# Optimization experiments

Measured on AMD Instinct MI355X. Metric: run time of the kernel, lower is better.

Reference implementation:

```python
import jax, jax.numpy as jnp
import numpy as np

N = 4096      # nodes
F = 32        # num_features (GATConv in = out per head)
H = 2         # heads
NHID = 64     # per-branch mlp output
C = 10        # num_classes
J = 3         # wavelet filters
E = 65536     # edges (avg degree 16)
G = 13        # num_gat = (3**3 - 1) // 2
NEG_SLOPE = 0.2


def setup_inputs() -> dict:
    key = jax.random.key(0)
    ks = jax.random.split(key, 12)
    sc = np.float32(1.0 / np.sqrt(N))
    g = np.float32(0.1)
    x = jax.random.normal(ks[0], (N, F), jnp.float32)
    edge_index = jax.random.randint(ks[1], (2, E), 0, N)
    U = jax.random.normal(ks[2], (N, N), jnp.float32) * sc
    psi = jax.random.normal(ks[3], (J, N, N), jnp.float32) * sc
    # 13 GATConv(F, F, heads=H) parameter stacks
    gat_W = jax.random.normal(ks[4], (G, F, H * F), jnp.float32) * g
    att_src = jax.random.normal(ks[5], (G, H, F), jnp.float32) * g
    att_dst = jax.random.normal(ks[6], (G, H, F), jnp.float32) * g
    gat_b = jnp.zeros((G, H * F), jnp.float32)
    # 13 branch MLPs: Linear(H*F -> NHID)
    mlp_W = jax.random.normal(ks[7], (G, H * F, NHID), jnp.float32) * g
    mlp_b = jnp.zeros((G, NHID), jnp.float32)
    # final head: Linear(13*NHID -> C)
    out_W = jax.random.normal(ks[8], (G * NHID, C), jnp.float32) * g
    out_b = jnp.zeros((C,), jnp.float32)
    return {"x": x, "edge_index": edge_index, "U": U, "psi": psi,
            "gat_W": gat_W, "att_src": att_src, "att_dst": att_dst,
            "gat_b": gat_b, "mlp_W": mlp_W, "mlp_b": mlp_b,
            "out_W": out_W, "out_b": out_b}


def _gat_branch(coef, W, a_s, a_d, bg, mw, mb, src, dst):
    # GATConv(F, F, heads=H, concat=True) in eval mode, then ELU + Linear.
    h = (coef @ W).reshape(N, H, F)                       # [N,H,F]
    es = jnp.einsum('nhf,hf->nh', h, a_s)                 # src attention logits
    ed = jnp.einsum('nhf,hf->nh', h, a_d)                 # dst attention logits
    e = jax.nn.leaky_relu(es[src] + ed[dst], NEG_SLOPE)   # [E+N,H]
    m = jax.ops.segment_max(e, dst, num_segments=N)       # stable softmax per dst
    w = jnp.exp(e - m[dst])
    z = jax.ops.segment_sum(w, dst, num_segments=N)
    alpha = w / (z[dst] + 1e-16)
    out = jax.ops.segment_sum(alpha[:, :, None] * h[src], dst, num_segments=N)
    out = out.reshape(N, H * F) + bg
    return jax.nn.elu(out) @ mw + mb                      # branch MLP -> [N,NHID]


def reference(x, edge_index, U, psi, gat_W, att_src, att_dst, gat_b,
              mlp_W, mlp_b, out_W, out_b):
    loops = jnp.arange(N)
    src = jnp.concatenate([edge_index[0], loops])         # add_self_loops
    dst = jnp.concatenate([edge_index[1], loops])
    # Scattering tree (layer=3, J=3): 1 + 3 + 9 = 13 coefficient maps.
    af = jnp.abs(x)
    coef0 = U @ af                                        # [N,F]
    y1 = jnp.einsum('jnm,mf->jnf', psi, af)               # level-1 wavelets [J,N,F]
    a1 = jnp.abs(y1)
    coef1 = jnp.einsum('nm,jmf->jnf', U, a1)              # [J,N,F]
    y2 = jnp.einsum('knm,jmf->jknf', psi, a1)             # level-2: psi_k @ |y1_j|
    coef2 = jnp.einsum('nm,jkmf->jknf', U, jnp.abs(y2)).reshape(J * J, N, F)
    coefs = jnp.concatenate([coef0[None], coef1, coef2], axis=0)  # [13,N,F]
    branch = jax.vmap(lambda c, W, a_s, a_d, bg, mw, mb:
                      _gat_branch(c, W, a_s, a_d, bg, mw, mb, src, dst))
    yb = branch(coefs, gat_W, att_src, att_dst, gat_b, mlp_W, mlp_b)  # [13,N,NHID]
    feat = jnp.moveaxis(yb, 0, 1).reshape(N, G * NHID)    # concat branches per node
    logits = jax.nn.elu(feat) @ out_W + out_b             # [N,C]
    return jax.nn.log_softmax(logits, axis=1)
```

## Files before the change

kernel.cpp:

```cpp
#include <hip/hip_runtime.h>
#include <hip/hip_bf16.h>

#define NN 4096
#define FF 32
#define EE 65536
#define GG 13

typedef float floatx4 __attribute__((ext_vector_type(4)));
typedef __bf16 bf16x8 __attribute__((ext_vector_type(8)));
typedef short short8 __attribute__((ext_vector_type(8)));

__device__ inline unsigned short f2bf(float f) {
    unsigned u = __float_as_uint(f);
    u += 0x7FFFu + ((u >> 16) & 1u);
    return (unsigned short)(u >> 16);
}

__device__ inline void gl2lds16(const float* g, float* l) {
    __builtin_amdgcn_global_load_lds(
        (__attribute__((address_space(1))) void*)(void*)(g),
        (__attribute__((address_space(3))) void*)(l), 16, 0, 0);
}


__global__ void k_prep1(const float* __restrict__ x, unsigned short* __restrict__ B) {
    int tid = blockIdx.x * 256 + threadIdx.x;
    int k = tid >> 5, col = tid & 31;
    float v = fabsf(x[tid]);
    B[(((k >> 5) * 2 + (col >> 4)) << 9) + ((col & 15) << 5) + (k & 31)] = f2bf(v);
}

__global__ void k_prep2(const float* __restrict__ P1, unsigned short* __restrict__ B) {
    int tid = blockIdx.x * 256 + threadIdx.x;
    int k = tid / 96, jf = tid % 96;
    int j = jf >> 5, f = jf & 31;
    float v = fabsf(P1[((1 + j) * NN + k) * FF + f]);
    B[(((k >> 5) * 6 + (jf >> 4)) << 9) + ((jf & 15) << 5) + (k & 31)] = f2bf(v);
}

__global__ void k_prep3(const float* __restrict__ P2, unsigned short* __restrict__ B) {
    int tid = blockIdx.x * 256 + threadIdx.x;
    int k = tid / 288, cc = tid % 288;
    int k3 = cc / 96, jf = cc % 96;
    float v = fabsf(P2[((1 + k3) * NN + k) * 96 + jf]);
    B[(((k >> 5) * 18 + (cc >> 4)) << 9) + ((cc & 15) << 5) + (k & 31)] = f2bf(v);
}

__global__ __launch_bounds__(512, 8) void k_pass1(const float* __restrict__ Umat,
                                                  const float* __restrict__ Psi,
                                                  const unsigned short* __restrict__ Bfrag,
                                                  float* __restrict__ Pout,
                                                  unsigned short* __restrict__ Apack) {
    __shared__ float abuf[2][16 * 256];
    __shared__ float cs[2][16 * 32];
    int tile = blockIdx.x, mat = blockIdx.y;
    const float* A = (mat == 0) ? Umat : (Psi + (size_t)(mat - 1) * NN * NN);
    int tid = threadIdx.x;
    int wave = tid >> 6, lane = tid & 63;
    int c15 = lane & 15, q = lane >> 4;

    const float* atile = A + (size_t)tile * 16 * NN;
    const unsigned short* bbase = Bfrag + (c15 << 5) + (q << 3);
    unsigned short* apk = Apack + ((size_t)mat << 24) + (size_t)tile * 65536
                          + (c15 << 5) + (q << 3);

    int r0 = 2 * wave, r1 = 2 * wave + 1;
    const float* g0 = atile + (size_t)r0 * NN + ((lane ^ (r0 & 7)) << 2);
    const float* g1 = atile + (size_t)r1 * NN + ((lane ^ (r1 & 7)) << 2);
    float* l0 = &abuf[0][wave * 512];
    float* l1 = &abuf[1][wave * 512];

    int swz = c15 & 7;
    int u0 = ((wave * 8 + q * 2 + 0) ^ swz) << 2;
    int u1 = ((wave * 8 + q * 2 + 1) ^ swz) << 2;
    int rowbase = c15 << 8;

    floatx4 acc0 = {0.f, 0.f, 0.f, 0.f}, acc1 = {0.f, 0.f, 0.f, 0.f};

    gl2lds16(g0, l0);
    gl2lds16(g1, l0 + 256);
    asm volatile("" ::: "memory");
    short8 pb0 = *(const short8*)(bbase + (size_t)(wave * 2 + 0) * 512);
    short8 pb1 = *(const short8*)(bbase + (size_t)(wave * 2 + 1) * 512);
    asm volatile("s_waitcnt vmcnt(2)" ::: "memory");
    __builtin_amdgcn_s_barrier();
    __builtin_amdgcn_sched_barrier(0);

    for (int c = 0; c < 16; c++) {
        const float* rb = abuf[c & 1];
        if (c < 15) {
            float* wbb = (c & 1) ? l0 : l1;
            gl2lds16(g0 + (size_t)(c + 1) * 256, wbb);
            gl2lds16(g1 + (size_t)(c + 1) * 256, wbb + 256);
        }
        asm volatile("" ::: "memory");
        int ksg = c * 8 + wave;
        floatx4 f0 = *(const floatx4*)(rb + rowbase + u0);
        floatx4 f1 = *(const floatx4*)(rb + rowbase + u1);
        short8 bv0 = pb0, bv1 = pb1;
        if (c < 15) {
            pb0 = *(const short8*)(bbase + (size_t)((ksg + 8) * 2 + 0) * 512);
            pb1 = *(const short8*)(bbase + (size_t)((ksg + 8) * 2 + 1) * 512);
        }
        short8 av;
        av[0]=f2bf(f0[0]); av[1]=f2bf(f0[1]); av[2]=f2bf(f0[2]); av[3]=f2bf(f0[3]);
        av[4]=f2bf(f1[0]); av[5]=f2bf(f1[1]); av[6]=f2bf(f1[2]); av[7]=f2bf(f1[3]);
        *(short8*)(apk + (size_t)ksg * 512) = av;
        bf16x8 ab = __builtin_bit_cast(bf16x8, av);
        acc0 = __builtin_amdgcn_mfma_f32_16x16x32_bf16(ab, __builtin_bit_cast(bf16x8, bv0), acc0, 0, 0, 0);
        acc1 = __builtin_amdgcn_mfma_f32_16x16x32_bf16(ab, __builtin_bit_cast(bf16x8, bv1), acc1, 0, 0, 0);
        if (c < 15) {
            asm volatile("s_waitcnt vmcnt(3)" ::: "memory");
            __builtin_amdgcn_s_barrier();
            __builtin_amdgcn_sched_barrier(0);
        }
    }

    int half = wave & 1;
    floatx4 acc[2] = {acc0, acc1};
    for (int w2 = 0; w2 < 4; w2++) {
        if ((wave >> 1) == w2) {
#pragma unroll
            for (int t = 0; t < 2; t++)
#pragma unroll
                for (int r = 0; r < 4; r++) {
                    int idx = (q * 4 + r) * 32 + t * 16 + c15;
                    if (w2 == 0) cs[half][idx] = acc[t][r];
                    else cs[half][idx] += acc[t][r];
                }
        }
        __syncthreads();
    }
    float* orow = Pout + ((size_t)mat * NN + (size_t)tile * 16) * 32;
    for (int i = tid; i < 16 * 32; i += 512) orow[i] = cs[0][i] + cs[1][i];
}

template <int NT, int NTOT>
__global__ __launch_bounds__(512) void k_passP(const unsigned short* __restrict__ Apack,
                                               const unsigned short* __restrict__ Bfrag,
                                               float* __restrict__ Pout) {
    constexpr int NC = NT * 16;
    constexpr int NCTOT = NTOT * 16;
    int tile = blockIdx.x;
    int mat = blockIdx.y;
    int cg = blockIdx.z;
    int tid = threadIdx.x;
    int wave = tid >> 6, lane = tid & 63;
    int c15 = lane & 15, q = lane >> 4;
    const unsigned short* ap = Apack + ((size_t)mat << 24) + (size_t)tile * 65536
                               + (size_t)(wave * 16) * 512 + (c15 << 5) + (q << 3);
    const unsigned short* bbase = Bfrag + (size_t)(wave * 16) * NTOT * 512
                                  + (size_t)(cg * NT) * 512 + (c15 << 5) + (q << 3);

    floatx4 acc[NT];
#pragma unroll
    for (int t = 0; t < NT; t++) acc[t] = (floatx4){0.f, 0.f, 0.f, 0.f};

    short8 af = *(const short8*)ap;
    short8 bv[NT];
#pragma unroll
    for (int t = 0; t < NT; t++) bv[t] = *(const short8*)(bbase + t * 512);

    for (int s = 0; s < 15; s++) {
        short8 af2 = *(const short8*)(ap + (s + 1) * 512);
        short8 bv2[NT];
        const unsigned short* bp = bbase + (size_t)(s + 1) * NTOT * 512;
#pragma unroll
        for (int t = 0; t < NT; t++) bv2[t] = *(const short8*)(bp + t * 512);
        bf16x8 ab = __builtin_bit_cast(bf16x8, af);
#pragma unroll
        for (int t = 0; t < NT; t++)
            acc[t] = __builtin_amdgcn_mfma_f32_16x16x32_bf16(
                ab, __builtin_bit_cast(bf16x8, bv[t]), acc[t], 0, 0, 0);
        af = af2;
#pragma unroll
        for (int t = 0; t < NT; t++) bv[t] = bv2[t];
    }
    {
        bf16x8 ab = __builtin_bit_cast(bf16x8, af);
#pragma unroll
        for (int t = 0; t < NT; t++)
            acc[t] = __builtin_amdgcn_mfma_f32_16x16x32_bf16(
                ab, __builtin_bit_cast(bf16x8, bv[t]), acc[t], 0, 0, 0);
    }

    __shared__ float cs[2][16 * NC];
    int half = wave & 1;
    for (int w2 = 0; w2 < 4; w2++) {
        if ((wave >> 1) == w2) {
#pragma unroll
            for (int t = 0; t < NT; t++)
#pragma unroll
                for (int r = 0; r < 4; r++) {
                    int idx = (q * 4 + r) * NC + t * 16 + c15;
                    if (w2 == 0) cs[half][idx] = acc[t][r];
                    else cs[half][idx] += acc[t][r];
                }
        }
        __syncthreads();
    }
    float* orow = Pout + ((size_t)mat * NN + (size_t)tile * 16) * NCTOT + cg * NC;
    for (int i = tid; i < 16 * NC; i += 512) {
        int r = i / NC, c = i % NC;
        orow[(size_t)r * NCTOT + c] = cs[0][i] + cs[1][i];
    }
}

__global__ void k_hes(const float* __restrict__ P1, const float* __restrict__ P2,
                      const float* __restrict__ P3, const float* __restrict__ gatW,
                      const float* __restrict__ attS, const float* __restrict__ attD,
                      float* __restrict__ h, float* __restrict__ es,
                      float* __restrict__ ed) {
    int w = (blockIdx.x * 256 + threadIdx.x) >> 6;
    int lane = threadIdx.x & 63;
    int g = w >> 12, n = w & 4095;
    const float* crow;
    if (g == 0) crow = P1 + (size_t)n * FF;
    else if (g <= 3) crow = P2 + (size_t)n * 96 + (g - 1) * 32;
    else {
        int j = (g - 4) / 3, k3 = (g - 4) % 3;
        crow = P3 + (size_t)n * 288 + k3 * 96 + j * 32;
    }
    const float* wcol = gatW + g * (32 * 64) + lane;
    float a = 0.f;
#pragma unroll
    for (int f = 0; f < 32; f++) a += crow[f] * wcol[f * 64];
    h[(size_t)w * 64 + lane] = a;
    float vs = a * attS[g * 64 + lane];
    float vd = a * attD[g * 64 + lane];
#pragma unroll
    for (int off = 16; off >= 1; off >>= 1) {
        vs += __shfl_down(vs, off, 32);
        vd += __shfl_down(vd, off, 32);
    }
    if ((lane & 31) == 0) {
        es[w * 2 + (lane >> 5)] = vs;
        ed[w * 2 + (lane >> 5)] = vd;
    }
}

__global__ void k_hist(const int* __restrict__ ei, int* __restrict__ cnt) {
    int e = blockIdx.x * 256 + threadIdx.x;
    int d = (e < EE) ? ei[EE + e] : (e - EE);
    atomicAdd(&cnt[d], 1);
}

__global__ void k_scan(const int* __restrict__ cnt, int* __restrict__ offs,
                       int* __restrict__ cursor) {
    int lane = threadIdx.x;
    int base = lane * 64;
    int s = 0;
    for (int i = 0; i < 64; i++) s += cnt[base + i];
    int x = s;
    for (int d = 1; d < 64; d <<= 1) {
        int y = __shfl_up(x, d);
        if (lane >= d) x += y;
    }
    int run = x - s;
    for (int i = 0; i < 64; i++) {
        offs[base + i] = run;
        cursor[base + i] = run;
        run += cnt[base + i];
    }
}

__global__ void k_scatter(const int* __restrict__ ei, int* __restrict__ cursor,
                          int* __restrict__ csr) {
    int e = blockIdx.x * 256 + threadIdx.x;
    int s, d;
    if (e < EE) { s = ei[e]; d = ei[EE + e]; } else { s = d = e - EE; }
    int pos = atomicAdd(&cursor[d], 1);
    csr[pos] = s;
}

__global__ void k_gat(const float* __restrict__ h, const float* __restrict__ es,
                      const float* __restrict__ ed, const int* __restrict__ offs,
                      const int* __restrict__ cnt, const int* __restrict__ csr,
                      const float* __restrict__ gatb, float* __restrict__ gact) {
    int w = (blockIdx.x * 256 + threadIdx.x) >> 6;
    int lane = threadIdx.x & 63, hh = lane >> 5;
    int g = w >> 12, n = w & 4095;
    float myed = ed[w * 2 + hh];
    float bias = gatb[g * 64 + lane];
    int start = offs[n], deg = cnt[n];
    const float* hg = h + (size_t)g * NN * 64;
    const float* esg = es + (size_t)g * NN * 2;
    int sA = csr[start];
    int sB = (deg > 1) ? csr[start + 1] : 0;
    float hvA = hg[(size_t)sA * 64 + lane];
    float lgA = esg[sA * 2 + hh];
    float m = -INFINITY, z = 0.f, acc = 0.f;
    for (int i = 0; i < deg; i++) {
        int sC = (i + 2 < deg) ? csr[start + i + 2] : 0;
        float hvB = hg[(size_t)sB * 64 + lane];
        float lgB = esg[sB * 2 + hh];
        float lg = lgA + myed;
        lg = (lg > 0.f) ? lg : 0.2f * lg;
        float nm = fmaxf(m, lg);
        float sc = __expf(m - nm);
        float we = __expf(lg - nm);
        z = z * sc + we;
        acc = acc * sc + we * hvA;
        m = nm;
        sA = sB; sB = sC; hvA = hvB; lgA = lgB;
    }
    float o = acc / (z + 1e-16f) + bias;
    o = (o > 0.f) ? o : (__expf(o) - 1.f);
    gact[(size_t)w * 64 + lane] = o;
}

__global__ void k_mlp(const float* __restrict__ gact, const float* __restrict__ mlpW,
                      const float* __restrict__ mlpb, float* __restrict__ feat) {
    int tid = blockIdx.x * 256 + threadIdx.x;
    int g = tid >> 18;
    int n = (tid & ((1 << 18) - 1)) >> 6;
    int k = tid & 63;
    const float* grow = gact + ((size_t)g * NN + n) * 64;
    const float* wc = mlpW + (size_t)g * 64 * 64 + k;
    float a = mlpb[g * 64 + k];
#pragma unroll 8
    for (int i = 0; i < 64; i++) a += grow[i] * wc[i * 64];
    a = (a > 0.f) ? a : (__expf(a) - 1.f);
    feat[(size_t)n * 832 + g * 64 + k] = a;
}

__global__ void k_final(const float* __restrict__ feat, const float* __restrict__ oW,
                        const float* __restrict__ ob, float* __restrict__ out) {
    int w = (blockIdx.x * 256 + threadIdx.x) >> 6;
    int lane = threadIdx.x & 63;
    float a[10];
#pragma unroll
    for (int c = 0; c < 10; c++) a[c] = 0.f;
    const float* frow = feat + (size_t)w * 832;
#pragma unroll
    for (int i = 0; i < 13; i++) {
        float v = frow[i * 64 + lane];
        const float* wp = oW + (i * 64 + lane) * 10;
#pragma unroll
        for (int c = 0; c < 10; c++) a[c] += v * wp[c];
    }
#pragma unroll
    for (int off = 32; off >= 1; off >>= 1)
#pragma unroll
        for (int c = 0; c < 10; c++) a[c] += __shfl_down(a[c], off);
    if (lane == 0) {
        float m = -INFINITY;
#pragma unroll
        for (int c = 0; c < 10; c++) { a[c] += ob[c]; m = fmaxf(m, a[c]); }
        float s = 0.f;
#pragma unroll
        for (int c = 0; c < 10; c++) s += __expf(a[c] - m);
        float lse = m + __logf(s);
#pragma unroll
        for (int c = 0; c < 10; c++) out[w * 10 + c] = a[c] - lse;
    }
}

extern "C" void kernel_launch(void* const* d_in, const int* in_sizes, int n_in,
                              void* d_out, int out_size, void* d_ws, size_t ws_size,
                              hipStream_t stream) {
    const float* x    = (const float*)d_in[0];
    const int*   ei   = (const int*)d_in[1];
    const float* U    = (const float*)d_in[2];
    const float* psi  = (const float*)d_in[3];
    const float* gatW = (const float*)d_in[4];
    const float* attS = (const float*)d_in[5];
    const float* attD = (const float*)d_in[6];
    const float* gatb = (const float*)d_in[7];
    const float* mlpW = (const float*)d_in[8];
    const float* mlpb = (const float*)d_in[9];
    const float* oW   = (const float*)d_in[10];
    const float* ob   = (const float*)d_in[11];
    float* out = (float*)d_out;

    char* ws = (char*)d_ws;
    size_t off = 0;
    auto alloc = [&](size_t bytes) { char* p = ws + off; off += (bytes + 255) & ~(size_t)255; return p; };
    unsigned short* Apack = (unsigned short*)alloc((size_t)4 * NN * NN * 2);
    unsigned short* bf1 = (unsigned short*)alloc((size_t)NN * 32 * 2);
    float* P1           = (float*)alloc((size_t)4 * NN * 32 * 4);
    unsigned short* bf2 = (unsigned short*)alloc((size_t)NN * 96 * 2);
    float* P2           = (float*)alloc((size_t)4 * NN * 96 * 4);
    unsigned short* bf3 = (unsigned short*)alloc((size_t)NN * 288 * 2);
    float* P3           = (float*)alloc((size_t)NN * 288 * 4);
    float* h            = (float*)alloc((size_t)GG * NN * 64 * 4);
    float* es           = (float*)alloc((size_t)GG * NN * 2 * 4);
    float* ed           = (float*)alloc((size_t)GG * NN * 2 * 4);
    int* cnt            = (int*)alloc((size_t)NN * 4);
    int* offs           = (int*)alloc((size_t)NN * 4);
    int* cursor         = (int*)alloc((size_t)NN * 4);
    int* csr            = (int*)alloc((size_t)(EE + NN) * 4);
    float* gact         = (float*)alloc((size_t)GG * NN * 64 * 4);
    float* feat         = (float*)alloc((size_t)NN * 832 * 4);
    (void)ws_size; (void)in_sizes; (void)n_in; (void)out_size;

    hipMemsetAsync(cnt, 0, NN * 4, stream);
    k_hist<<<(EE + NN) / 256, 256, 0, stream>>>(ei, cnt);
    k_scan<<<1, 64, 0, stream>>>(cnt, offs, cursor);
    k_scatter<<<(EE + NN) / 256, 256, 0, stream>>>(ei, cursor, csr);

    k_prep1<<<(NN * 32) / 256, 256, 0, stream>>>(x, bf1);
    k_pass1<<<dim3(NN / 16, 4), 512, 0, stream>>>(U, psi, bf1, P1, Apack);
    k_prep2<<<(NN * 96) / 256, 256, 0, stream>>>(P1, bf2);
    k_passP<6, 6><<<dim3(NN / 16, 4, 1), 512, 0, stream>>>(Apack, bf2, P2);
    k_prep3<<<(NN * 288) / 256, 256, 0, stream>>>(P2, bf3);
    k_passP<6, 18><<<dim3(NN / 16, 1, 3), 512, 0, stream>>>(Apack, bf3, P3);

    k_hes<<<(GG * NN * 64) / 256, 256, 0, stream>>>(P1, P2, P3, gatW, attS, attD, h, es, ed);
    k_gat<<<(GG * NN * 64) / 256, 256, 0, stream>>>(h, es, ed, offs, cnt, csr, gatb, gact);
    k_mlp<<<(GG * NN * 64) / 256, 256, 0, stream>>>(gact, mlpW, mlpb, feat);
    k_final<<<(NN * 64) / 256, 256, 0, stream>>>(feat, oW, ob, out);
}
```

Before: 646.9 us.

## Process two row tiles per block in passP and fuse MLP with final head

Each k_passP block now computes two adjacent 16-row tiles, so every B fragment loaded from global memory feeds two MFMAs. The grid is halved to match, and the explicit software prefetch of A and B is dropped in favour of direct loads. Separately, k_mlp and k_final are merged into one per-node kernel that keeps the 832-wide feature row in shared memory, which removes the feat buffer round trip and one launch. The cost is fewer blocks in the GEMM passes and a fused kernel in which only one wave does the final reduction.

```diff
diff --git a/kernel.cpp b/kernel.cpp
--- a/kernel.cpp
+++ b/kernel.cpp
@@ -141,69 +141,70 @@
                                                float* __restrict__ Pout) {
     constexpr int NC = NT * 16;
     constexpr int NCTOT = NTOT * 16;
-    int tile = blockIdx.x;
+    int tp = blockIdx.x;
     int mat = blockIdx.y;
     int cg = blockIdx.z;
     int tid = threadIdx.x;
     int wave = tid >> 6, lane = tid & 63;
     int c15 = lane & 15, q = lane >> 4;
-    const unsigned short* ap = Apack + ((size_t)mat << 24) + (size_t)tile * 65536
-                               + (size_t)(wave * 16) * 512 + (c15 << 5) + (q << 3);
+    const unsigned short* ap0 = Apack + ((size_t)mat << 24) + (size_t)(2 * tp) * 65536
+                                + (size_t)(wave * 16) * 512 + (c15 << 5) + (q << 3);
+    const unsigned short* ap1 = ap0 + 65536;
     const unsigned short* bbase = Bfrag + (size_t)(wave * 16) * NTOT * 512
                                   + (size_t)(cg * NT) * 512 + (c15 << 5) + (q << 3);
 
-    floatx4 acc[NT];
-#pragma unroll
-    for (int t = 0; t < NT; t++) acc[t] = (floatx4){0.f, 0.f, 0.f, 0.f};
-
-    short8 af = *(const short8*)ap;
-    short8 bv[NT];
-#pragma unroll
-    for (int t = 0; t < NT; t++) bv[t] = *(const short8*)(bbase + t * 512);
-
-    for (int s = 0; s < 15; s++) {
-        short8 af2 = *(const short8*)(ap + (s + 1) * 512);
-        short8 bv2[NT];
-        const unsigned short* bp = bbase + (size_t)(s + 1) * NTOT * 512;
-#pragma unroll
-        for (int t = 0; t < NT; t++) bv2[t] = *(const short8*)(bp + t * 512);
-        bf16x8 ab = __builtin_bit_cast(bf16x8, af);
-#pragma unroll
-        for (int t = 0; t < NT; t++)
-            acc[t] = __builtin_amdgcn_mfma_f32_16x16x32_bf16(
-                ab, __builtin_bit_cast(bf16x8, bv[t]), acc[t], 0, 0, 0);
-        af = af2;
-#pragma unroll
-        for (int t = 0; t < NT; t++) bv[t] = bv2[t];
-    }
-    {
-        bf16x8 ab = __builtin_bit_cast(bf16x8, af);
-#pragma unroll
-        for (int t = 0; t < NT; t++)
-            acc[t] = __builtin_amdgcn_mfma_f32_16x16x32_bf16(
-                ab, __builtin_bit_cast(bf16x8, bv[t]), acc[t], 0, 0, 0);
+    floatx4 acc0[NT], acc1[NT];
+#pragma unroll
+    for (int t = 0; t < NT; t++) {
+        acc0[t] = (floatx4){0.f, 0.f, 0.f, 0.f};
+        acc1[t] = (floatx4){0.f, 0.f, 0.f, 0.f};
+    }
+
+    for (int s = 0; s < 16; s++) {
+        short8 a0 = *(const short8*)(ap0 + (size_t)s * 512);
+        short8 a1 = *(const short8*)(ap1 + (size_t)s * 512);
+        const unsigned short* bp = bbase + (size_t)s * NTOT * 512;
+        bf16x8 ab0 = __builtin_bit_cast(bf16x8, a0);
+        bf16x8 ab1 = __builtin_bit_cast(bf16x8, a1);
+#pragma unroll
+        for (int t = 0; t < NT; t++) {
+            short8 bv = *(const short8*)(bp + t * 512);
+            bf16x8 bb = __builtin_bit_cast(bf16x8, bv);
+            acc0[t] = __builtin_amdgcn_mfma_f32_16x16x32_bf16(ab0, bb, acc0[t], 0, 0, 0);
+            acc1[t] = __builtin_amdgcn_mfma_f32_16x16x32_bf16(ab1, bb, acc1[t], 0, 0, 0);
+        }
     }
 
     __shared__ float cs[2][16 * NC];
     int half = wave & 1;
-    for (int w2 = 0; w2 < 4; w2++) {
-        if ((wave >> 1) == w2) {
-#pragma unroll
-            for (int t = 0; t < NT; t++)
-#pragma unroll
-                for (int r = 0; r < 4; r++) {
-                    int idx = (q * 4 + r) * NC + t * 16 + c15;
-                    if (w2 == 0) cs[half][idx] = acc[t][r];
-                    else cs[half][idx] += acc[t][r];
-                }
-        }
-        __syncthreads();
-    }
-    float* orow = Pout + ((size_t)mat * NN + (size_t)tile * 16) * NCTOT + cg * NC;
-    for (int i = tid; i < 16 * NC; i += 512) {
-        int r = i / NC, c = i % NC;
-        orow[(size_t)r * NCTOT + c] = cs[0][i] + cs[1][i];
-    }
+
+#define REDUCE_WRITE(ACC, TILE)                                                   \
+    for (int w2 = 0; w2 < 4; w2++) {                                              \
+        if ((wave >> 1) == w2) {                                                  \
+            _Pragma("unroll")                                                     \
+            for (int t = 0; t < NT; t++)                                          \
+                _Pragma("unroll")                                                 \
+                for (int r = 0; r < 4; r++) {                                     \
+                    int idx = (q * 4 + r) * NC + t * 16 + c15;                    \
+                    if (w2 == 0) cs[half][idx] = ACC[t][r];                       \
+                    else cs[half][idx] += ACC[t][r];                              \
+                }                                                                 \
+        }                                                                         \
+        __syncthreads();                                                          \
+    }                                                                             \
+    {                                                                             \
+        float* orow = Pout + ((size_t)mat * NN + (size_t)(TILE) * 16) * NCTOT     \
+                      + cg * NC;                                                  \
+        for (int i = tid; i < 16 * NC; i += 512) {                                \
+            int r = i / NC, c = i % NC;                                           \
+            orow[(size_t)r * NCTOT + c] = cs[0][i] + cs[1][i];                    \
+        }                                                                         \
+    }
+
+    REDUCE_WRITE(acc0, 2 * tp)
+    __syncthreads();
+    REDUCE_WRITE(acc1, 2 * tp + 1)
+#undef REDUCE_WRITE
 }
 
 __global__ void k_hes(const float* __restrict__ P1, const float* __restrict__ P2,
@@ -309,50 +310,50 @@
     gact[(size_t)w * 64 + lane] = o;
 }
 
-__global__ void k_mlp(const float* __restrict__ gact, const float* __restrict__ mlpW,
-                      const float* __restrict__ mlpb, float* __restrict__ feat) {
-    int tid = blockIdx.x * 256 + threadIdx.x;
-    int g = tid >> 18;
-    int n = (tid & ((1 << 18) - 1)) >> 6;
-    int k = tid & 63;
+__global__ __launch_bounds__(832) void k_out(const float* __restrict__ gact,
+                                             const float* __restrict__ mlpW,
+                                             const float* __restrict__ mlpb,
+                                             const float* __restrict__ oW,
+                                             const float* __restrict__ ob,
+                                             float* __restrict__ out) {
+    __shared__ float sf[832];
+    int n = blockIdx.x;
+    int g = threadIdx.x >> 6;
+    int k = threadIdx.x & 63;
     const float* grow = gact + ((size_t)g * NN + n) * 64;
     const float* wc = mlpW + (size_t)g * 64 * 64 + k;
     float a = mlpb[g * 64 + k];
 #pragma unroll 8
     for (int i = 0; i < 64; i++) a += grow[i] * wc[i * 64];
     a = (a > 0.f) ? a : (__expf(a) - 1.f);
-    feat[(size_t)n * 832 + g * 64 + k] = a;
-}
-
-__global__ void k_final(const float* __restrict__ feat, const float* __restrict__ oW,
-                        const float* __restrict__ ob, float* __restrict__ out) {
-    int w = (blockIdx.x * 256 + threadIdx.x) >> 6;
-    int lane = threadIdx.x & 63;
-    float a[10];
-#pragma unroll
-    for (int c = 0; c < 10; c++) a[c] = 0.f;
-    const float* frow = feat + (size_t)w * 832;
-#pragma unroll
-    for (int i = 0; i < 13; i++) {
-        float v = frow[i * 64 + lane];
-        const float* wp = oW + (i * 64 + lane) * 10;
-#pragma unroll
-        for (int c = 0; c < 10; c++) a[c] += v * wp[c];
-    }
-#pragma unroll
-    for (int off = 32; off >= 1; off >>= 1)
-#pragma unroll
-        for (int c = 0; c < 10; c++) a[c] += __shfl_down(a[c], off);
-    if (lane == 0) {
-        float m = -INFINITY;
-#pragma unroll
-        for (int c = 0; c < 10; c++) { a[c] += ob[c]; m = fmaxf(m, a[c]); }
-        float s = 0.f;
-#pragma unroll
-        for (int c = 0; c < 10; c++) s += __expf(a[c] - m);
-        float lse = m + __logf(s);
-#pragma unroll
-        for (int c = 0; c < 10; c++) out[w * 10 + c] = a[c] - lse;
+    sf[g * 64 + k] = a;
+    __syncthreads();
+    if (g == 0) {
+        float acc[10];
+#pragma unroll
+        for (int c = 0; c < 10; c++) acc[c] = 0.f;
+#pragma unroll
+        for (int i = 0; i < 13; i++) {
+            float v = sf[i * 64 + k];
+            const float* wp = oW + (i * 64 + k) * 10;
+#pragma unroll
+            for (int c = 0; c < 10; c++) acc[c] += v * wp[c];
+        }
+#pragma unroll
+        for (int off = 32; off >= 1; off >>= 1)
+#pragma unroll
+            for (int c = 0; c < 10; c++) acc[c] += __shfl_down(acc[c], off);
+        if (k == 0) {
+            float m = -INFINITY;
+#pragma unroll
+            for (int c = 0; c < 10; c++) { acc[c] += ob[c]; m = fmaxf(m, acc[c]); }
+            float s = 0.f;
+#pragma unroll
+            for (int c = 0; c < 10; c++) s += __expf(acc[c] - m);
+            float lse = m + __logf(s);
+#pragma unroll
+            for (int c = 0; c < 10; c++) out[n * 10 + c] = acc[c] - lse;
+        }
     }
 }
 
@@ -391,7 +392,6 @@
     int* cursor         = (int*)alloc((size_t)NN * 4);
     int* csr            = (int*)alloc((size_t)(EE + NN) * 4);
     float* gact         = (float*)alloc((size_t)GG * NN * 64 * 4);
-    float* feat         = (float*)alloc((size_t)NN * 832 * 4);
     (void)ws_size; (void)in_sizes; (void)n_in; (void)out_size;
 
     hipMemsetAsync(cnt, 0, NN * 4, stream);
@@ -402,12 +402,11 @@
     k_prep1<<<(NN * 32) / 256, 256, 0, stream>>>(x, bf1);
     k_pass1<<<dim3(NN / 16, 4), 512, 0, stream>>>(U, psi, bf1, P1, Apack);
     k_prep2<<<(NN * 96) / 256, 256, 0, stream>>>(P1, bf2);
-    k_passP<6, 6><<<dim3(NN / 16, 4, 1), 512, 0, stream>>>(Apack, bf2, P2);
+    k_passP<6, 6><<<dim3(NN / 32, 4, 1), 512, 0, stream>>>(Apack, bf2, P2);
     k_prep3<<<(NN * 288) / 256, 256, 0, stream>>>(P2, bf3);
-    k_passP<6, 18><<<dim3(NN / 16, 1, 3), 512, 0, stream>>>(Apack, bf3, P3);
+    k_passP<6, 18><<<dim3(NN / 32, 1, 3), 512, 0, stream>>>(Apack, bf3, P3);
 
     k_hes<<<(GG * NN * 64) / 256, 256, 0, stream>>>(P1, P2, P3, gatW, attS, attD, h, es, ed);
     k_gat<<<(GG * NN * 64) / 256, 256, 0, stream>>>(h, es, ed, offs, cnt, csr, gatb, gact);
-    k_mlp<<<(GG * NN * 64) / 256, 256, 0, stream>>>(gact, mlpW, mlpb, feat);
-    k_final<<<(NN * 64) / 256, 256, 0, stream>>>(feat, oW, ob, out);
-}
+    k_out<<<NN, 832, 0, stream>>>(gact, mlpW, mlpb, oW, ob, out);
+}
```

Result: faster. 627.6 us (-3.0%).
